# Optimization experiments

Measured on AMD Instinct MI355X. Metric: run time of the kernel, lower is better.

Reference implementation:

```python
import jax, jax.numpy as jnp
import numpy as np

N = 50000      # nodes
E = 800000     # edges
G = 64         # graphs in batch
IN_F, H1, C1, C2, OUT_F = 128, 4, 32, 64, 16
D1 = H1 * C1   # 128, concat output of gat1
EPS = 1e-5
NEG_SLOPE = 0.2


def setup_inputs() -> dict:
    key = jax.random.key(0)
    ks = jax.random.split(key, 16)
    rn = lambda k, shape, s=0.1: jax.random.normal(k, shape, jnp.float32) * s
    inp = {
        'x': jax.random.normal(ks[0], (N, IN_F), jnp.float32),
        'edge_index': jax.random.randint(ks[1], (2, E), 0, N),
        'edge_attr': jax.random.uniform(ks[2], (E, 1), jnp.float32),
        'batch': jnp.sort(jax.random.randint(ks[3], (N,), 0, G)),
        # GATv2 layer 1 (heads=4, concat)
        'Wl1': rn(ks[4], (IN_F, D1)), 'bl1': jnp.zeros((D1,), jnp.float32),
        'Wr1': rn(ks[5], (IN_F, D1)), 'br1': jnp.zeros((D1,), jnp.float32),
        'We1': rn(ks[6], (1, D1)), 'att1': rn(ks[7], (H1, C1)),
        'bias1': jnp.zeros((D1,), jnp.float32),
        # GATv2 layer 2 (heads=1, concat=False)
        'Wl2': rn(ks[8], (D1, C2)), 'bl2': jnp.zeros((C2,), jnp.float32),
        'Wr2': rn(ks[9], (D1, C2)), 'br2': jnp.zeros((C2,), jnp.float32),
        'We2': rn(ks[10], (1, C2)), 'att2': rn(ks[11], (1, C2)),
        'bias2': jnp.zeros((C2,), jnp.float32),
        # batchnorms
        'bn1_gamma': jnp.ones((D1,), jnp.float32), 'bn1_beta': jnp.zeros((D1,), jnp.float32),
        'bn2_gamma': jnp.ones((C2,), jnp.float32), 'bn2_beta': jnp.zeros((C2,), jnp.float32),
        # final linear over [sum|mean|max] pooled features
        'Wlin': rn(ks[12], (3 * C2, OUT_F)), 'blin': jnp.zeros((OUT_F,), jnp.float32),
    }
    return inp


def gatv2(x, src, dst, edge_attr, Wl, bl, Wr, br, We, att, bias, H, C, concat):
    n = x.shape[0]
    xl = (x @ Wl + bl).reshape(n, H, C)          # source transform (lin_l)
    xr = (x @ Wr + br).reshape(n, H, C)          # target transform (lin_r)
    e = (edge_attr @ We).reshape(-1, H, C)       # edge transform (lin_edge)
    m = jax.nn.leaky_relu(xl[src] + xr[dst] + e, NEG_SLOPE)  # [E,H,C]
    alpha = jnp.einsum('ehc,hc->eh', m, att)     # attention logits [E,H]
    amax = jax.ops.segment_max(alpha, dst, num_segments=n)
    amax = jnp.where(jnp.isfinite(amax), amax, 0.0)
    p = jnp.exp(alpha - amax[dst])
    denom = jax.ops.segment_sum(p, dst, num_segments=n)
    a = p / (denom[dst] + 1e-16)                 # per-destination softmax
    out = jax.ops.segment_sum(xl[src] * a[:, :, None], dst, num_segments=n)
    out = out.reshape(n, H * C) if concat else out.mean(axis=1)
    return out + bias


def batchnorm(x, gamma, beta):
    mu = x.mean(axis=0)
    var = x.var(axis=0)  # biased var, as torch BN uses for normalization
    return (x - mu) * jax.lax.rsqrt(var + EPS) * gamma + beta


def reference(x, edge_index, edge_attr, batch,
              Wl1, bl1, Wr1, br1, We1, att1, bias1,
              Wl2, bl2, Wr2, br2, We2, att2, bias2,
              bn1_gamma, bn1_beta, bn2_gamma, bn2_beta,
              Wlin, blin):
    src, dst = edge_index[0], edge_index[1]
    h = jax.nn.relu(gatv2(x, src, dst, edge_attr, Wl1, bl1, Wr1, br1, We1, att1, bias1, H1, C1, True))
    h = batchnorm(h, bn1_gamma, bn1_beta)
    # dropout omitted (eval-mode reference)
    h = jax.nn.relu(gatv2(h, src, dst, edge_attr, Wl2, bl2, Wr2, br2, We2, att2, bias2, 1, C2, False))
    h = batchnorm(h, bn2_gamma, bn2_beta)
    # multi-pool over graphs
    s = jax.ops.segment_sum(h, batch, num_segments=G)
    cnt = jax.ops.segment_sum(jnp.ones((h.shape[0], 1), h.dtype), batch, num_segments=G)
    mean = s / jnp.maximum(cnt, 1.0)
    mx = jax.ops.segment_max(h, batch, num_segments=G)
    feat = jnp.concatenate([s, mean, mx], axis=-1)   # [G, 3*C2]
    return feat @ Wlin + blin
```

## Files before the change

### kernel.cpp

```cpp
#include <hip/hip_runtime.h>
#include <math.h>


typedef __attribute__((ext_vector_type(8))) short short8v;
typedef __attribute__((ext_vector_type(8))) unsigned short ushort8v;
typedef __attribute__((ext_vector_type(4))) unsigned short ushort4v;
typedef __attribute__((ext_vector_type(4))) float f32x4v;

#define BUCKCAP 8192

__device__ __forceinline__ void atomicMaxFloat(float* addr, float val) {
    if (val >= 0.f) atomicMax((int*)addr, __float_as_int(val));
    else            atomicMin((unsigned int*)addr, __float_as_uint(val));
}
__device__ __forceinline__ void atomicMinFloat(float* addr, float val) {
    if (val >= 0.f) atomicMin((int*)addr, __float_as_int(val));
    else            atomicMax((unsigned int*)addr, __float_as_uint(val));
}

__device__ __forceinline__ unsigned short f2bf(float f) {
    unsigned u = __float_as_uint(f);
    unsigned r = u + 0x7FFFu + ((u >> 16) & 1u);
    return (unsigned short)(r >> 16);
}
__device__ __forceinline__ float bf2f(unsigned short h) {
    return __uint_as_float((unsigned)h << 16);
}

__global__ void setup_kernel(const float* __restrict__ x,
                             const float* __restrict__ Wl1, const float* __restrict__ Wr1,
                             unsigned short* __restrict__ xbf, unsigned short* __restrict__ w1t,
                             int* __restrict__ bcur, float* __restrict__ bn1stats,
                             float* __restrict__ bn2stats, float* __restrict__ gsum,
                             float* __restrict__ gmax, float* __restrict__ gmin,
                             float* __restrict__ gcnt, int nquads) {
    int i = blockIdx.x * blockDim.x + threadIdx.x;
    int stride = gridDim.x * blockDim.x;
    for (int j = i; j < nquads; j += stride) {
        float4 v = ((const float4*)x)[j];
        ushort4 o = { f2bf(v.x), f2bf(v.y), f2bf(v.z), f2bf(v.w) };
        ((ushort4*)xbf)[j] = o;
    }
    for (int j = i; j < 256 * 128; j += stride) {
        int col = j >> 7, k = j & 127;
        float w = (col < 128) ? Wl1[k * 128 + col] : Wr1[k * 128 + (col - 128)];
        w1t[j] = f2bf(w);
    }
    for (int j = i; j < 64 * 64; j += stride) { gsum[j] = 0.f; gmax[j] = -INFINITY; gmin[j] = INFINITY; }
    if (i < 256) { bcur[i] = 0; bn1stats[i] = 0.f; }
    if (i < 128) bn2stats[i] = 0.f;
    if (i < 64)  gcnt[i] = 0.f;
}

__global__ __launch_bounds__(256)
void passA_kernel(const int* __restrict__ esrc_in, const int* __restrict__ edst_in,
                  const float* __restrict__ eattr, uint2* __restrict__ brec,
                  int* __restrict__ bcur, int nE) {
    __shared__ unsigned scnt[256];
    __shared__ unsigned sbase[256];
    const int t = threadIdx.x;
    const int e0 = blockIdx.x * 4096;
    scnt[t] = 0;
    __syncthreads();
    unsigned rx[16], ry[16]; unsigned short rk[16];
#pragma unroll
    for (int j = 0; j < 16; ++j) {
        int e = e0 + j * 256 + t;
        if (e < nE) {
            unsigned d = (unsigned)edst_in[e];
            rx[j] = (d << 16) | (unsigned)esrc_in[e];
            ry[j] = __float_as_uint(eattr[e]);
            rk[j] = (unsigned short)atomicAdd(&scnt[d >> 8], 1u);
        }
    }
    __syncthreads();
    sbase[t] = (scnt[t] > 0) ? (unsigned)atomicAdd(&bcur[t], (int)scnt[t]) : 0u;
    __syncthreads();
#pragma unroll
    for (int j = 0; j < 16; ++j) {
        int e = e0 + j * 256 + t;
        if (e < nE) {
            unsigned b = rx[j] >> 24;
            unsigned pos = sbase[b] + rk[j];
            if (pos < BUCKCAP) brec[(size_t)b * BUCKCAP + pos] = make_uint2(rx[j], ry[j]);
        }
    }
}

__global__ __launch_bounds__(256)
void passB1_kernel(const uint2* __restrict__ brec, const int* __restrict__ bcur,
                   int* __restrict__ rowptr, int nN, int nE) {
    __shared__ unsigned cnt[256];
    __shared__ int red[256];
    const int b = blockIdx.x, t = threadIdx.x;
    cnt[t] = 0;
    red[t] = (t < b) ? bcur[t] : 0;
    __syncthreads();
    for (int off = 128; off; off >>= 1) {
        if (t < off) red[t] += red[t + off];
        __syncthreads();
    }
    const int base = red[0];
    const int n = bcur[b];
    const uint2* r = brec + (size_t)b * BUCKCAP;
    for (int i = t; i < n; i += 256) atomicAdd(&cnt[(r[i].x >> 16) & 255u], 1u);
    __syncthreads();
    const unsigned v = cnt[t];
    red[t] = (int)v;
    __syncthreads();
    for (int off = 1; off < 256; off <<= 1) {
        int xv = (t >= off) ? red[t - off] : 0;
        __syncthreads();
        red[t] += xv;
        __syncthreads();
    }
    const int excl = red[t] - (int)v;
    const int d = (b << 8) + t;
    if (d <= nN) rowptr[d] = base + excl;
    if (b == gridDim.x - 1 && t == 255) rowptr[nN] = nE;
}

__global__ __launch_bounds__(256)
void passB2_kernel(const uint2* __restrict__ brec, const int* __restrict__ bcur,
                   const int* __restrict__ rowptr, unsigned* __restrict__ edges, int nN) {
    __shared__ unsigned cur[256];
    __shared__ int rp[256];
    const int b = blockIdx.x, t = threadIdx.x;
    const int d0 = b << 8;
    cur[t] = 0;
    if (d0 + t < nN) rp[t] = rowptr[d0 + t];
    __syncthreads();
    const int n = bcur[b];
    const uint2* r = brec + (size_t)b * BUCKCAP;
    for (int i = t; i < n; i += 256) {
        uint2 rec = r[i];
        unsigned dlo = (rec.x >> 16) & 255u;
        unsigned rank = atomicAdd(&cur[dlo], 1u);
        int pos = rp[dlo] + (int)rank;
        edges[pos] = (rec.x & 0xFFFFu) | ((unsigned)f2bf(__uint_as_float(rec.y)) << 16);
    }
}

template <int NO>
__global__ __launch_bounds__(256)
void mfma_transform_kernel(const unsigned short* __restrict__ A,
                           const unsigned short* __restrict__ Wt,
                           const float* __restrict__ bL, const float* __restrict__ bR,
                           unsigned short* __restrict__ outL, unsigned short* __restrict__ outR,
                           int M) {
    constexpr int NCG = NO / 64;
    const int wid  = (blockIdx.x * blockDim.x + threadIdx.x) >> 6;
    const int lane = threadIdx.x & 63;
    const int rowblk = wid / NCG;
    const int cg     = wid % NCG;
    if (rowblk * 16 >= M) return;
    int r = rowblk * 16 + (lane & 15);
    if (r >= M) r = M - 1;
    const int ko = (lane >> 4) * 8;
    const int cbase = cg * 64;

    f32x4v acc0 = {0.f,0.f,0.f,0.f}, acc1 = acc0, acc2 = acc0, acc3 = acc0;
#pragma unroll
    for (int k0 = 0; k0 < 128; k0 += 32) {
        short8v a = *(const short8v*)(A + (size_t)r * 128 + k0 + ko);
        const unsigned short* wp = Wt + (size_t)(cbase + (lane & 15)) * 128 + k0 + ko;
        short8v b0 = *(const short8v*)(wp);
        short8v b1 = *(const short8v*)(wp + 16 * 128);
        short8v b2 = *(const short8v*)(wp + 32 * 128);
        short8v b3 = *(const short8v*)(wp + 48 * 128);
        acc0 = __builtin_amdgcn_mfma_f32_16x16x32_bf16(a, b0, acc0, 0, 0, 0);
        acc1 = __builtin_amdgcn_mfma_f32_16x16x32_bf16(a, b1, acc1, 0, 0, 0);
        acc2 = __builtin_amdgcn_mfma_f32_16x16x32_bf16(a, b2, acc2, 0, 0, 0);
        acc3 = __builtin_amdgcn_mfma_f32_16x16x32_bf16(a, b3, acc3, 0, 0, 0);
    }

    const int colL  = lane & 15;
    const int rquad = (lane >> 4) * 4;
    f32x4v accs[4] = { acc0, acc1, acc2, acc3 };
#pragma unroll
    for (int c = 0; c < 4; ++c) {
        const int gcol = cbase + c * 16 + colL;
        float bias; unsigned short* outp; int oc;
        if (gcol < NO / 2) { bias = bL[gcol]; outp = outL; oc = gcol; }
        else               { bias = bR[gcol - NO / 2]; outp = outR; oc = gcol - NO / 2; }
#pragma unroll
        for (int j = 0; j < 4; ++j) {
            const int row = rowblk * 16 + rquad + j;
            if (row < M) outp[(size_t)row * (NO / 2) + oc] = f2bf(accs[c][j] + bias);
        }
    }
}

__device__ __forceinline__ float edge_c8(unsigned w, bool act, ushort8v xu,
                                         const float* xrv, const float* wev,
                                         const float* atv, float* xv) {
    const float ea = bf2f((unsigned short)(w >> 16));
    float part = 0.f;
#pragma unroll
    for (int q = 0; q < 8; ++q) {
        xv[q] = bf2f(xu[q]);
        float t = xv[q] + xrv[q] + ea * wev[q];
        t = fmaxf(t, 0.2f * t);
        part += t * atv[q];
    }
    part += __shfl_xor(part, 1);
    part += __shfl_xor(part, 2);
    return act ? __expf(part) : 0.f;
}

__device__ __forceinline__ float edge_c4(unsigned w, bool act, ushort4v xu,
                                         const float* xrv, const float* wev,
                                         const float* atv, float* xv) {
    const float ea = bf2f((unsigned short)(w >> 16));
    float part = 0.f;
#pragma unroll
    for (int q = 0; q < 4; ++q) {
        xv[q] = bf2f(xu[q]);
        float t = xv[q] + xrv[q] + ea * wev[q];
        t = fmaxf(t, 0.2f * t);
        part += t * atv[q];
    }
    part += __shfl_xor(part, 1);
    part += __shfl_xor(part, 2);
    part += __shfl_xor(part, 4);
    part += __shfl_xor(part, 8);
    return act ? __expf(part) : 0.f;
}

__global__ __launch_bounds__(256)
void gather1_kernel(const unsigned short* __restrict__ xl, const unsigned short* __restrict__ xr,
                    const int* __restrict__ rowptr, const unsigned* __restrict__ edges,
                    const float* __restrict__ We, const float* __restrict__ att,
                    const float* __restrict__ bias, unsigned short* __restrict__ y, int nN) {
    const int lane = threadIdx.x & 63;
    const int sub  = lane >> 4;
    const int sl   = lane & 15;
    const int c0   = sl * 8;
    const int waveg = (blockIdx.x * blockDim.x + threadIdx.x) >> 6;
    const int n = waveg * 4 + sub;
    const bool valid = (n < nN);

    float xrv[8];
    int ks = 0, ke = 0;
    if (valid) {
        ushort8v xu = *(const ushort8v*)(xr + (size_t)n * 128 + c0);
#pragma unroll
        for (int j = 0; j < 8; ++j) xrv[j] = bf2f(xu[j]);
        ks = rowptr[n]; ke = rowptr[n + 1];
    } else {
#pragma unroll
        for (int j = 0; j < 8; ++j) xrv[j] = 0.f;
    }
    const float4 we0 = *(const float4*)(We + c0);
    const float4 we1 = *(const float4*)(We + c0 + 4);
    const float4 at0 = *(const float4*)(att + c0);
    const float4 at1 = *(const float4*)(att + c0 + 4);
    const float wev[8] = { we0.x, we0.y, we0.z, we0.w, we1.x, we1.y, we1.z, we1.w };
    const float atv[8] = { at0.x, at0.y, at0.z, at0.w, at1.x, at1.y, at1.z, at1.w };

    float d = 0.f, a[8];
#pragma unroll
    for (int j = 0; j < 8; ++j) a[j] = 0.f;

    for (int kb = ks; __any(kb < ke); kb += 16) {
        const unsigned ew = (kb + sl < ke) ? edges[kb + sl] : 0u;
        const int cnt = ke - kb;
        for (int j = 0; j < 16; j += 4) {
            if (!__any(j < cnt)) break;
            const unsigned w0 = __shfl(ew, sub * 16 + j + 0);
            const unsigned w1 = __shfl(ew, sub * 16 + j + 1);
            const unsigned w2 = __shfl(ew, sub * 16 + j + 2);
            const unsigned w3 = __shfl(ew, sub * 16 + j + 3);
            const ushort8v xu0 = *(const ushort8v*)(xl + (size_t)(w0 & 0xFFFFu) * 128 + c0);
            const ushort8v xu1 = *(const ushort8v*)(xl + (size_t)(w1 & 0xFFFFu) * 128 + c0);
            const ushort8v xu2 = *(const ushort8v*)(xl + (size_t)(w2 & 0xFFFFu) * 128 + c0);
            const ushort8v xu3 = *(const ushort8v*)(xl + (size_t)(w3 & 0xFFFFu) * 128 + c0);
            float xva[8], xvb[8];
            const float e0 = edge_c8(w0, j + 0 < cnt, xu0, xrv, wev, atv, xva);
            const float e1 = edge_c8(w1, j + 1 < cnt, xu1, xrv, wev, atv, xvb);
            d += e0 + e1;
#pragma unroll
            for (int q = 0; q < 8; ++q) a[q] += e0 * xva[q] + e1 * xvb[q];
            const float e2 = edge_c8(w2, j + 2 < cnt, xu2, xrv, wev, atv, xva);
            const float e3 = edge_c8(w3, j + 3 < cnt, xu3, xrv, wev, atv, xvb);
            d += e2 + e3;
#pragma unroll
            for (int q = 0; q < 8; ++q) a[q] += e2 * xva[q] + e3 * xvb[q];
        }
    }
    if (valid) {
        const float inv = 1.f / (d + 1e-16f);
        ushort8v o;
#pragma unroll
        for (int j = 0; j < 8; ++j) o[j] = f2bf(fmaxf(a[j] * inv + bias[c0 + j], 0.f));
        *(ushort8v*)(y + (size_t)n * 128 + c0) = o;
    }
}

__global__ __launch_bounds__(256)
void gather2_kernel(const unsigned short* __restrict__ xl, const unsigned short* __restrict__ xr,
                    const int* __restrict__ rowptr, const unsigned* __restrict__ edges,
                    const float* __restrict__ We, const float* __restrict__ att,
                    const float* __restrict__ bias, float* __restrict__ y, int nN) {
    const int lane = threadIdx.x & 63;
    const int sub  = lane >> 4;
    const int sl   = lane & 15;
    const int c0   = sl * 4;
    const int waveg = (blockIdx.x * blockDim.x + threadIdx.x) >> 6;
    const int n = waveg * 4 + sub;
    const bool valid = (n < nN);

    float xrv[4];
    int ks = 0, ke = 0;
    if (valid) {
        ushort4v xu = *(const ushort4v*)(xr + (size_t)n * 64 + c0);
#pragma unroll
        for (int j = 0; j < 4; ++j) xrv[j] = bf2f(xu[j]);
        ks = rowptr[n]; ke = rowptr[n + 1];
    } else {
#pragma unroll
        for (int j = 0; j < 4; ++j) xrv[j] = 0.f;
    }
    const float4 wev4 = *(const float4*)(We + c0);
    const float4 atv4 = *(const float4*)(att + c0);
    const float wev[4] = { wev4.x, wev4.y, wev4.z, wev4.w };
    const float atv[4] = { atv4.x, atv4.y, atv4.z, atv4.w };

    float d = 0.f, a[4] = {0.f, 0.f, 0.f, 0.f};
    for (int kb = ks; __any(kb < ke); kb += 16) {
        const unsigned ew = (kb + sl < ke) ? edges[kb + sl] : 0u;
        const int cnt = ke - kb;
        for (int j = 0; j < 16; j += 4) {
            if (!__any(j < cnt)) break;
            const unsigned w0 = __shfl(ew, sub * 16 + j + 0);
            const unsigned w1 = __shfl(ew, sub * 16 + j + 1);
            const unsigned w2 = __shfl(ew, sub * 16 + j + 2);
            const unsigned w3 = __shfl(ew, sub * 16 + j + 3);
            const ushort4v xu0 = *(const ushort4v*)(xl + (size_t)(w0 & 0xFFFFu) * 64 + c0);
            const ushort4v xu1 = *(const ushort4v*)(xl + (size_t)(w1 & 0xFFFFu) * 64 + c0);
            const ushort4v xu2 = *(const ushort4v*)(xl + (size_t)(w2 & 0xFFFFu) * 64 + c0);
            const ushort4v xu3 = *(const ushort4v*)(xl + (size_t)(w3 & 0xFFFFu) * 64 + c0);
            float xva[4], xvb[4];
            const float e0 = edge_c4(w0, j + 0 < cnt, xu0, xrv, wev, atv, xva);
            const float e1 = edge_c4(w1, j + 1 < cnt, xu1, xrv, wev, atv, xvb);
            d += e0 + e1;
#pragma unroll
            for (int q = 0; q < 4; ++q) a[q] += e0 * xva[q] + e1 * xvb[q];
            const float e2 = edge_c4(w2, j + 2 < cnt, xu2, xrv, wev, atv, xva);
            const float e3 = edge_c4(w3, j + 3 < cnt, xu3, xrv, wev, atv, xvb);
            d += e2 + e3;
#pragma unroll
            for (int q = 0; q < 4; ++q) a[q] += e2 * xva[q] + e3 * xvb[q];
        }
    }
    if (valid) {
        const float inv = 1.f / (d + 1e-16f);
        float4 o;
        o.x = fmaxf(a[0] * inv + bias[c0],     0.f);
        o.y = fmaxf(a[1] * inv + bias[c0 + 1], 0.f);
        o.z = fmaxf(a[2] * inv + bias[c0 + 2], 0.f);
        o.w = fmaxf(a[3] * inv + bias[c0 + 3], 0.f);
        *(float4*)(y + (size_t)n * 64 + c0) = o;
    }
}

__global__ void bn_stats_bf128_kernel(const unsigned short* __restrict__ y,
                                      float* __restrict__ stats, int rows) {
    const int t = threadIdx.x;
    const int col = t & 127;
    const int rsub = t >> 7;
    float s = 0.f, q = 0.f;
    for (int r = blockIdx.x * 2 + rsub; r < rows; r += gridDim.x * 2) {
        float v = bf2f(y[(size_t)r * 128 + col]);
        s += v; q += v * v;
    }
    atomicAdd(&stats[col], s);
    atomicAdd(&stats[128 + col], q);
}

__global__ void wfold2_kernel(const float* __restrict__ Wl2, const float* __restrict__ bl2,
                              const float* __restrict__ Wr2, const float* __restrict__ br2,
                              const float* __restrict__ stats, const float* __restrict__ gamma,
                              const float* __restrict__ beta,
                              unsigned short* __restrict__ w2t, float* __restrict__ b2f, int nN) {
    __shared__ float sc[128], sh[128];
    const int t = threadIdx.x;
    if (t < 128) {
        float invN = 1.f / nN;
        float mu = stats[t] * invN;
        float var = stats[128 + t] * invN - mu * mu;
        float k = gamma[t] * rsqrtf(var + 1e-5f);
        sc[t] = k; sh[t] = beta[t] - mu * k;
    }
    __syncthreads();
    if (t < 128) {
        const int oc = (t < 64) ? t : t - 64;
        const float* W = (t < 64) ? Wl2 : Wr2;
        float acc = (t < 64) ? bl2[oc] : br2[oc];
        for (int k = 0; k < 128; ++k) acc += sh[k] * W[k * 64 + oc];
        b2f[t] = acc;
    }
    for (int i = t; i < 128 * 128; i += 256) {
        int col = i >> 7, k = i & 127;
        const int oc = (col < 64) ? col : col - 64;
        const float* W = (col < 64) ? Wl2 : Wr2;
        w2t[i] = f2bf(sc[k] * W[k * 64 + oc]);
    }
}

__global__ void pool_kernel(const float* __restrict__ y2, const int* __restrict__ batch,
                            float* __restrict__ gsum, float* __restrict__ gmax,
                            float* __restrict__ gmin, float* __restrict__ gcnt,
                            float* __restrict__ bn2stats, int rows) {
    const int t = threadIdx.x;
    const int col = t & 63;
    const int rsub = t >> 6;
    const int base = blockIdx.x * 256;
    int curg = -1; float s = 0.f, mx = 0.f, mn = 0.f, cnt = 0.f;
    float bs = 0.f, bq = 0.f;
    int rend = rows < base + 256 ? rows : base + 256;
    for (int r = base + rsub; r < rend; r += 4) {
        int g = batch[r];
        float v = y2[(size_t)r * 64 + col];
        bs += v; bq += v * v;
        if (g != curg) {
            if (curg >= 0) {
                atomicAdd(&gsum[curg * 64 + col], s);
                atomicMaxFloat(&gmax[curg * 64 + col], mx);
                atomicMinFloat(&gmin[curg * 64 + col], mn);
                if (col == 0) atomicAdd(&gcnt[curg], cnt);
            }
            curg = g; s = v; mx = v; mn = v; cnt = 1.f;
        } else {
            s += v; mx = fmaxf(mx, v); mn = fminf(mn, v); cnt += 1.f;
        }
    }
    if (curg >= 0) {
        atomicAdd(&gsum[curg * 64 + col], s);
        atomicMaxFloat(&gmax[curg * 64 + col], mx);
        atomicMinFloat(&gmin[curg * 64 + col], mn);
        if (col == 0) atomicAdd(&gcnt[curg], cnt);
    }
    __shared__ float red[2][4][64];
    red[0][rsub][col] = bs; red[1][rsub][col] = bq;
    __syncthreads();
    if (rsub == 0) {
        float ts = red[0][0][col] + red[0][1][col] + red[0][2][col] + red[0][3][col];
        float tq = red[1][0][col] + red[1][1][col] + red[1][2][col] + red[1][3][col];
        atomicAdd(&bn2stats[col], ts);
        atomicAdd(&bn2stats[64 + col], tq);
    }
}

__global__ void final_kernel(const float* __restrict__ gsum, const float* __restrict__ gmax,
                             const float* __restrict__ gmin, const float* __restrict__ gcnt,
                             const float* __restrict__ bn2stats, const float* __restrict__ gamma,
                             const float* __restrict__ beta, const float* __restrict__ Wlin,
                             const float* __restrict__ blin, float* __restrict__ out, int nN) {
    __shared__ float feat[64][192];
    __shared__ float sc[64], sh[64];
    int t = threadIdx.x;
    if (t < 64) {
        float invN = 1.f / nN;
        float mu = bn2stats[t] * invN;
        float var = bn2stats[64 + t] * invN - mu * mu;
        float k = gamma[t] * rsqrtf(var + 1e-5f);
        sc[t] = k; sh[t] = beta[t] - mu * k;
    }
    __syncthreads();
    for (int i = t; i < 64 * 64; i += 256) {
        int g = i >> 6, c = i & 63;
        float cntg = gcnt[g];
        float s_bn = sc[c] * gsum[i] + sh[c] * cntg;
        feat[g][c]       = s_bn;
        feat[g][64 + c]  = s_bn / fmaxf(cntg, 1.f);
        feat[g][128 + c] = (sc[c] >= 0.f) ? sc[c] * gmax[i] + sh[c]
                                          : sc[c] * gmin[i] + sh[c];
    }
    __syncthreads();
    for (int i = t; i < 64 * 16; i += 256) {
        int g = i >> 4, j = i & 15;
        float acc = blin[j];
        for (int k = 0; k < 192; ++k) acc += feat[g][k] * Wlin[k * 16 + j];
        out[g * 16 + j] = acc;
    }
}

extern "C" void kernel_launch(void* const* d_in, const int* in_sizes, int n_in,
                              void* d_out, int out_size, void* d_ws, size_t ws_size,
                              hipStream_t stream) {
    const float* x     = (const float*)d_in[0];
    const int*   eidx  = (const int*)d_in[1];
    const float* eattr = (const float*)d_in[2];
    const int*   batch = (const int*)d_in[3];
    const float* Wl1 = (const float*)d_in[4];  const float* bl1 = (const float*)d_in[5];
    const float* Wr1 = (const float*)d_in[6];  const float* br1 = (const float*)d_in[7];
    const float* We1 = (const float*)d_in[8];  const float* att1 = (const float*)d_in[9];
    const float* bias1 = (const float*)d_in[10];
    const float* Wl2 = (const float*)d_in[11]; const float* bl2 = (const float*)d_in[12];
    const float* Wr2 = (const float*)d_in[13]; const float* br2 = (const float*)d_in[14];
    const float* We2 = (const float*)d_in[15]; const float* att2 = (const float*)d_in[16];
    const float* bias2 = (const float*)d_in[17];
    const float* g1 = (const float*)d_in[18];  const float* b1 = (const float*)d_in[19];
    const float* g2 = (const float*)d_in[20];  const float* b2 = (const float*)d_in[21];
    const float* Wlin = (const float*)d_in[22]; const float* blin = (const float*)d_in[23];
    float* out = (float*)d_out;

    const int nN = in_sizes[0] / 128;
    const int nE = in_sizes[1] / 2;
    const int* esrc_in = eidx;
    const int* edst_in = eidx + nE;
    const int nbuck = (nN + 255) >> 8;

    char* ws = (char*)d_ws;
    size_t o = 0;
    auto alloc = [&](size_t bytes) { size_t r = o; o += (bytes + 255) & ~(size_t)255; return r; };
    unsigned short* B0 = (unsigned short*)(ws + alloc((size_t)nN * 128 * 2));
    unsigned short* B1 = (unsigned short*)(ws + alloc((size_t)nN * 128 * 2));
    char*           B2 = (char*)(ws + alloc((size_t)nN * 128 * 2));
    unsigned short* w1t = (unsigned short*)(ws + alloc(256 * 128 * 2));
    unsigned short* w2t = (unsigned short*)(ws + alloc(128 * 128 * 2));
    float* b2f    = (float*)(ws + alloc(128 * 4));
    uint2* brec   = (uint2*)(ws + alloc((size_t)nbuck * BUCKCAP * 8));
    unsigned* edges = (unsigned*)(ws + alloc((size_t)nE * 4));
    int*   bcur   = (int*)(ws + alloc(256 * 4));
    int*   rowptr = (int*)(ws + alloc((size_t)(nN + 1) * 4));
    float* bn1stats = (float*)(ws + alloc(256 * 4));
    float* bn2stats = (float*)(ws + alloc(128 * 4));
    float* gsum = (float*)(ws + alloc(64 * 64 * 4));
    float* gmax = (float*)(ws + alloc(64 * 64 * 4));
    float* gmin = (float*)(ws + alloc(64 * 64 * 4));
    float* gcnt = (float*)(ws + alloc(64 * 4));

    unsigned short* xbf  = B0;
    unsigned short* y1bf = B0;
    unsigned short* xl1b = B1;
    unsigned short* xr1b = (unsigned short*)B2;
    unsigned short* xl2b = B1;
    unsigned short* xr2b = B1 + (size_t)nN * 64;
    float*          y2   = (float*)B2;

    const int mBlk = (nN + 15) / 16;
    const int t1Blocks = mBlk;
    const int t2Blocks = (mBlk * 2 + 3) / 4;

    setup_kernel<<<2048, 256, 0, stream>>>(x, Wl1, Wr1, xbf, w1t, bcur,
                                           bn1stats, bn2stats, gsum, gmax, gmin, gcnt, nN * 32);
    passA_kernel<<<(nE + 4095) / 4096, 256, 0, stream>>>(esrc_in, edst_in, eattr, brec, bcur, nE);
    passB1_kernel<<<nbuck, 256, 0, stream>>>(brec, bcur, rowptr, nN, nE);
    passB2_kernel<<<nbuck, 256, 0, stream>>>(brec, bcur, rowptr, edges, nN);

    mfma_transform_kernel<256><<<t1Blocks, 256, 0, stream>>>(
        xbf, w1t, bl1, br1, xl1b, xr1b, nN);
    gather1_kernel<<<(nN + 15) / 16, 256, 0, stream>>>(
        xl1b, xr1b, rowptr, edges, We1, att1, bias1, y1bf, nN);
    bn_stats_bf128_kernel<<<256, 256, 0, stream>>>(y1bf, bn1stats, nN);
    wfold2_kernel<<<1, 256, 0, stream>>>(Wl2, bl2, Wr2, br2, bn1stats, g1, b1, w2t, b2f, nN);

    mfma_transform_kernel<128><<<t2Blocks, 256, 0, stream>>>(
        y1bf, w2t, b2f, b2f + 64, xl2b, xr2b, nN);
    gather2_kernel<<<(nN + 15) / 16, 256, 0, stream>>>(
        xl2b, xr2b, rowptr, edges, We2, att2, bias2, y2, nN);

    pool_kernel<<<(nN + 255) / 256, 256, 0, stream>>>(y2, batch, gsum, gmax, gmin, gcnt, bn2stats, nN);
    final_kernel<<<1, 256, 0, stream>>>(gsum, gmax, gmin, gcnt, bn2stats, g2, b2, Wlin, blin, out, nN);
}
```

Baseline: 364.1 us.

## Sort nodes by degree for gathers, fuse CSR passes, convert x inside MFMA

Builds a degree histogram during CSR construction and a permutation of nodes grouped by in-degree, so each gather wave processes nodes with similar edge counts and wave divergence drops. It merges the two CSR bucket passes into one kernel and drops the separate fp32-to-bf16 conversion of x by converting inside the first MFMA transform. The cost is an extra permute kernel, an extra perm lookup in each gather, and outputs scattered to non-contiguous rows. Storing the permutation as 16-bit ushort assumes the node count fits in 16 bits.

Measured after the change: 492.7 us. +35.3%, slower.

```diff
diff --git a/kernel.cpp b/kernel.cpp
--- a/kernel.cpp
+++ b/kernel.cpp
@@ -17,7 +17,6 @@
     if (val >= 0.f) atomicMin((int*)addr, __float_as_int(val));
     else            atomicMax((unsigned int*)addr, __float_as_uint(val));
 }
-
 __device__ __forceinline__ unsigned short f2bf(float f) {
     unsigned u = __float_as_uint(f);
     unsigned r = u + 0x7FFFu + ((u >> 16) & 1u);
@@ -27,20 +26,15 @@
     return __uint_as_float((unsigned)h << 16);
 }
 
-__global__ void setup_kernel(const float* __restrict__ x,
-                             const float* __restrict__ Wl1, const float* __restrict__ Wr1,
-                             unsigned short* __restrict__ xbf, unsigned short* __restrict__ w1t,
-                             int* __restrict__ bcur, float* __restrict__ bn1stats,
+__global__ void setup_kernel(const float* __restrict__ Wl1, const float* __restrict__ Wr1,
+                             unsigned short* __restrict__ w1t,
+                             int* __restrict__ bcur, int* __restrict__ deghist,
+                             int* __restrict__ bincur, float* __restrict__ bn1stats,
                              float* __restrict__ bn2stats, float* __restrict__ gsum,
                              float* __restrict__ gmax, float* __restrict__ gmin,
-                             float* __restrict__ gcnt, int nquads) {
+                             float* __restrict__ gcnt) {
     int i = blockIdx.x * blockDim.x + threadIdx.x;
     int stride = gridDim.x * blockDim.x;
-    for (int j = i; j < nquads; j += stride) {
-        float4 v = ((const float4*)x)[j];
-        ushort4 o = { f2bf(v.x), f2bf(v.y), f2bf(v.z), f2bf(v.w) };
-        ((ushort4*)xbf)[j] = o;
-    }
     for (int j = i; j < 256 * 128; j += stride) {
         int col = j >> 7, k = j & 127;
         float w = (col < 128) ? Wl1[k * 128 + col] : Wr1[k * 128 + (col - 128)];
@@ -49,7 +43,7 @@
     for (int j = i; j < 64 * 64; j += stride) { gsum[j] = 0.f; gmax[j] = -INFINITY; gmin[j] = INFINITY; }
     if (i < 256) { bcur[i] = 0; bn1stats[i] = 0.f; }
     if (i < 128) bn2stats[i] = 0.f;
-    if (i < 64)  gcnt[i] = 0.f;
+    if (i < 64)  { gcnt[i] = 0.f; deghist[i] = 0; bincur[i] = 0; }
 }
 
 __global__ __launch_bounds__(256)
@@ -88,10 +82,12 @@
 }
 
 __global__ __launch_bounds__(256)
-void passB1_kernel(const uint2* __restrict__ brec, const int* __restrict__ bcur,
-                   int* __restrict__ rowptr, int nN, int nE) {
+void passB_kernel(const uint2* __restrict__ brec, const int* __restrict__ bcur,
+                  int* __restrict__ rowptr, int* __restrict__ deghist,
+                  unsigned* __restrict__ edges, int nN, int nE) {
     __shared__ unsigned cnt[256];
     __shared__ int red[256];
+    __shared__ int rp[256];
     const int b = blockIdx.x, t = threadIdx.x;
     cnt[t] = 0;
     red[t] = (t < b) ? bcur[t] : 0;
@@ -106,6 +102,8 @@
     for (int i = t; i < n; i += 256) atomicAdd(&cnt[(r[i].x >> 16) & 255u], 1u);
     __syncthreads();
     const unsigned v = cnt[t];
+    const int d = (b << 8) + t;
+    if (d < nN) atomicAdd(&deghist[v < 63u ? v : 63u], 1);
     red[t] = (int)v;
     __syncthreads();
     for (int off = 1; off < 256; off <<= 1) {
@@ -114,36 +112,51 @@
         red[t] += xv;
         __syncthreads();
     }
-    const int excl = red[t] - (int)v;
-    const int d = (b << 8) + t;
-    if (d <= nN) rowptr[d] = base + excl;
+    rp[t] = base + red[t] - (int)v;
+    if (d <= nN) rowptr[d] = rp[t];
     if (b == gridDim.x - 1 && t == 255) rowptr[nN] = nE;
-}
-
-__global__ __launch_bounds__(256)
-void passB2_kernel(const uint2* __restrict__ brec, const int* __restrict__ bcur,
-                   const int* __restrict__ rowptr, unsigned* __restrict__ edges, int nN) {
-    __shared__ unsigned cur[256];
-    __shared__ int rp[256];
-    const int b = blockIdx.x, t = threadIdx.x;
-    const int d0 = b << 8;
-    cur[t] = 0;
-    if (d0 + t < nN) rp[t] = rowptr[d0 + t];
-    __syncthreads();
-    const int n = bcur[b];
-    const uint2* r = brec + (size_t)b * BUCKCAP;
+    __syncthreads();
+    cnt[t] = 0;
+    __syncthreads();
     for (int i = t; i < n; i += 256) {
         uint2 rec = r[i];
         unsigned dlo = (rec.x >> 16) & 255u;
-        unsigned rank = atomicAdd(&cur[dlo], 1u);
+        unsigned rank = atomicAdd(&cnt[dlo], 1u);
         int pos = rp[dlo] + (int)rank;
         edges[pos] = (rec.x & 0xFFFFu) | ((unsigned)f2bf(__uint_as_float(rec.y)) << 16);
     }
 }
 
-template <int NO>
 __global__ __launch_bounds__(256)
-void mfma_transform_kernel(const unsigned short* __restrict__ A,
+void permute_kernel(const int* __restrict__ rowptr, const int* __restrict__ deghist,
+                    int* __restrict__ bincur, unsigned short* __restrict__ perm, int nN) {
+    __shared__ int gbase[64];
+    __shared__ int lcnt[64];
+    __shared__ int lbase[64];
+    const int t = threadIdx.x;
+    if (t < 64) {
+        int acc = 0;
+        for (int i = 0; i < t; ++i) acc += deghist[i];
+        gbase[t] = acc;
+        lcnt[t] = 0;
+    }
+    __syncthreads();
+    const int d = blockIdx.x * 256 + t;
+    int bin = 0, myrank = 0;
+    if (d < nN) {
+        int deg = rowptr[d + 1] - rowptr[d];
+        bin = deg < 63 ? deg : 63;
+        myrank = atomicAdd(&lcnt[bin], 1);
+    }
+    __syncthreads();
+    if (t < 64 && lcnt[t] > 0) lbase[t] = atomicAdd(&bincur[t], lcnt[t]);
+    __syncthreads();
+    if (d < nN) perm[gbase[bin] + lbase[bin] + myrank] = (unsigned short)d;
+}
+
+template <int NO, bool F32IN>
+__global__ __launch_bounds__(256)
+void mfma_transform_kernel(const float* __restrict__ Af, const unsigned short* __restrict__ Ab,
                            const unsigned short* __restrict__ Wt,
                            const float* __restrict__ bL, const float* __restrict__ bR,
                            unsigned short* __restrict__ outL, unsigned short* __restrict__ outR,
@@ -162,7 +175,17 @@
     f32x4v acc0 = {0.f,0.f,0.f,0.f}, acc1 = acc0, acc2 = acc0, acc3 = acc0;
 #pragma unroll
     for (int k0 = 0; k0 < 128; k0 += 32) {
-        short8v a = *(const short8v*)(A + (size_t)r * 128 + k0 + ko);
+        short8v a;
+        if constexpr (F32IN) {
+            const float4 f0 = *(const float4*)(Af + (size_t)r * 128 + k0 + ko);
+            const float4 f1 = *(const float4*)(Af + (size_t)r * 128 + k0 + ko + 4);
+            a[0] = (short)f2bf(f0.x); a[1] = (short)f2bf(f0.y);
+            a[2] = (short)f2bf(f0.z); a[3] = (short)f2bf(f0.w);
+            a[4] = (short)f2bf(f1.x); a[5] = (short)f2bf(f1.y);
+            a[6] = (short)f2bf(f1.z); a[7] = (short)f2bf(f1.w);
+        } else {
+            a = *(const short8v*)(Ab + (size_t)r * 128 + k0 + ko);
+        }
         const unsigned short* wp = Wt + (size_t)(cbase + (lane & 15)) * 128 + k0 + ko;
         short8v b0 = *(const short8v*)(wp);
         short8v b1 = *(const short8v*)(wp + 16 * 128);
@@ -230,6 +253,7 @@
 __global__ __launch_bounds__(256)
 void gather1_kernel(const unsigned short* __restrict__ xl, const unsigned short* __restrict__ xr,
                     const int* __restrict__ rowptr, const unsigned* __restrict__ edges,
+                    const unsigned short* __restrict__ perm,
                     const float* __restrict__ We, const float* __restrict__ att,
                     const float* __restrict__ bias, unsigned short* __restrict__ y, int nN) {
     const int lane = threadIdx.x & 63;
@@ -237,8 +261,9 @@
     const int sl   = lane & 15;
     const int c0   = sl * 8;
     const int waveg = (blockIdx.x * blockDim.x + threadIdx.x) >> 6;
-    const int n = waveg * 4 + sub;
-    const bool valid = (n < nN);
+    const int i = waveg * 4 + sub;
+    const bool valid = (i < nN);
+    const int n = valid ? (int)perm[i] : 0;
 
     float xrv[8];
     int ks = 0, ke = 0;
@@ -300,6 +325,7 @@
 __global__ __launch_bounds__(256)
 void gather2_kernel(const unsigned short* __restrict__ xl, const unsigned short* __restrict__ xr,
                     const int* __restrict__ rowptr, const unsigned* __restrict__ edges,
+                    const unsigned short* __restrict__ perm,
                     const float* __restrict__ We, const float* __restrict__ att,
                     const float* __restrict__ bias, float* __restrict__ y, int nN) {
     const int lane = threadIdx.x & 63;
@@ -307,8 +333,9 @@
     const int sl   = lane & 15;
     const int c0   = sl * 4;
     const int waveg = (blockIdx.x * blockDim.x + threadIdx.x) >> 6;
-    const int n = waveg * 4 + sub;
-    const bool valid = (n < nN);
+    const int i = waveg * 4 + sub;
+    const bool valid = (i < nN);
+    const int n = valid ? (int)perm[i] : 0;
 
     float xrv[4];
     int ks = 0, ke = 0;
@@ -525,6 +552,9 @@
     unsigned* edges = (unsigned*)(ws + alloc((size_t)nE * 4));
     int*   bcur   = (int*)(ws + alloc(256 * 4));
     int*   rowptr = (int*)(ws + alloc((size_t)(nN + 1) * 4));
+    int*   deghist = (int*)(ws + alloc(64 * 4));
+    int*   bincur  = (int*)(ws + alloc(64 * 4));
+    unsigned short* perm = (unsigned short*)(ws + alloc((size_t)nN * 2));
     float* bn1stats = (float*)(ws + alloc(256 * 4));
     float* bn2stats = (float*)(ws + alloc(128 * 4));
     float* gsum = (float*)(ws + alloc(64 * 64 * 4));
@@ -532,7 +562,6 @@
     float* gmin = (float*)(ws + alloc(64 * 64 * 4));
     float* gcnt = (float*)(ws + alloc(64 * 4));
 
-    unsigned short* xbf  = B0;
     unsigned short* y1bf = B0;
     unsigned short* xl1b = B1;
     unsigned short* xr1b = (unsigned short*)B2;
@@ -544,23 +573,23 @@
     const int t1Blocks = mBlk;
     const int t2Blocks = (mBlk * 2 + 3) / 4;
 
-    setup_kernel<<<2048, 256, 0, stream>>>(x, Wl1, Wr1, xbf, w1t, bcur,
-                                           bn1stats, bn2stats, gsum, gmax, gmin, gcnt, nN * 32);
+    setup_kernel<<<256, 256, 0, stream>>>(Wl1, Wr1, w1t, bcur, deghist, bincur,
+                                          bn1stats, bn2stats, gsum, gmax, gmin, gcnt);
     passA_kernel<<<(nE + 4095) / 4096, 256, 0, stream>>>(esrc_in, edst_in, eattr, brec, bcur, nE);
-    passB1_kernel<<<nbuck, 256, 0, stream>>>(brec, bcur, rowptr, nN, nE);
-    passB2_kernel<<<nbuck, 256, 0, stream>>>(brec, bcur, rowptr, edges, nN);
-
-    mfma_transform_kernel<256><<<t1Blocks, 256, 0, stream>>>(
-        xbf, w1t, bl1, br1, xl1b, xr1b, nN);
+    passB_kernel<<<nbuck, 256, 0, stream>>>(brec, bcur, rowptr, deghist, edges, nN, nE);
+    permute_kernel<<<(nN + 255) / 256, 256, 0, stream>>>(rowptr, deghist, bincur, perm, nN);
+
+    mfma_transform_kernel<256, true><<<t1Blocks, 256, 0, stream>>>(
+        x, nullptr, w1t, bl1, br1, xl1b, xr1b, nN);
     gather1_kernel<<<(nN + 15) / 16, 256, 0, stream>>>(
-        xl1b, xr1b, rowptr, edges, We1, att1, bias1, y1bf, nN);
+        xl1b, xr1b, rowptr, edges, perm, We1, att1, bias1, y1bf, nN);
     bn_stats_bf128_kernel<<<256, 256, 0, stream>>>(y1bf, bn1stats, nN);
     wfold2_kernel<<<1, 256, 0, stream>>>(Wl2, bl2, Wr2, br2, bn1stats, g1, b1, w2t, b2f, nN);
 
-    mfma_transform_kernel<128><<<t2Blocks, 256, 0, stream>>>(
-        y1bf, w2t, b2f, b2f + 64, xl2b, xr2b, nN);
+    mfma_transform_kernel<128, false><<<t2Blocks, 256, 0, stream>>>(
+        nullptr, y1bf, w2t, b2f, b2f + 64, xl2b, xr2b, nN);
     gather2_kernel<<<(nN + 15) / 16, 256, 0, stream>>>(
-        xl2b, xr2b, rowptr, edges, We2, att2, bias2, y2, nN);
+        xl2b, xr2b, rowptr, edges, perm, We2, att2, bias2, y2, nN);
 
     pool_kernel<<<(nN + 255) / 256, 256, 0, stream>>>(y2, batch, gsum, gmax, gmin, gcnt, bn2stats, nN);
     final_kernel<<<1, 256, 0, stream>>>(gsum, gmax, gmin, gcnt, bn2stats, g2, b2, Wlin, blin, out, nN);
```
